# Kernel optimization log

Measured on AMD Instinct MI355X. Metric: run time of the kernel, lower is better.

The kernel has to match this reference:

```python
import jax, jax.numpy as jnp
import numpy as np

B, N, E, D = 4, 50000, 800000, 64


def setup_inputs() -> dict:
    key = jax.random.key(0)
    k_h, k_e, k_w1, k_w2 = jax.random.split(key, 4)
    s = 1.0 / np.sqrt(D)  # glorot-ish scale for 64x64 linear weights
    return {
        "t": jnp.zeros((1,), jnp.float32),
        "h": jax.random.normal(k_h, (B, N, D), jnp.float32),
        "edge_index": jax.random.randint(k_e, (2, E), 0, N, jnp.int32),
        "W1": jax.random.normal(k_w1, (D, D), jnp.float32) * s,
        "b1": jnp.zeros((D,), jnp.float32),
        "W2": jax.random.normal(k_w2, (D, D), jnp.float32) * s,
        "b2": jnp.zeros((D,), jnp.float32),
    }


def _gcn(x, row, col, norm, W, b, n_nodes):
    # x: (B, N, D). PyG GCNConv: linear (no bias) -> normalized gather/scatter -> +bias
    xw = jnp.einsum("bnd,de->bne", x, W)
    msg = xw[:, row, :] * norm[None, :, None]          # (B, E+N, D)
    agg = jax.vmap(lambda m: jax.ops.segment_sum(m, col, num_segments=n_nodes))(msg)
    return agg + b


def reference(t, h, edge_index, W1, b1, W2, b2):
    n_nodes = h.shape[1]
    loop = jnp.arange(n_nodes, dtype=edge_index.dtype)
    # add self-loops (PyG GCNConv default)
    row = jnp.concatenate([edge_index[0], loop])  # source nodes
    col = jnp.concatenate([edge_index[1], loop])  # target nodes
    # symmetric normalization D^{-1/2} (A+I) D^{-1/2}; degree counted on targets
    deg = jax.ops.segment_sum(jnp.ones_like(row, dtype=h.dtype), col, num_segments=n_nodes)
    dis = jnp.where(deg > 0, jax.lax.rsqrt(deg), 0.0)
    norm = dis[row] * dis[col]
    h = jnp.tanh(_gcn(h, row, col, norm, W1, b1, n_nodes))
    h = jnp.tanh(_gcn(h, row, col, norm, W2, b2, n_nodes))
    return h
```

## Files before the change

### kernel.cpp

```cpp
#include <hip/hip_runtime.h>
#include <math.h>

#define B_ 4
#define N_ 50000
#define E_ 800000
#define D_ 64
#define M_ (B_*N_)

typedef _Float16 h4 __attribute__((ext_vector_type(4)));
typedef _Float16 h8 __attribute__((ext_vector_type(8)));
typedef float    f4 __attribute__((ext_vector_type(4)));

__global__ __launch_bounds__(256) void k_count(const int4* __restrict__ col4, int* __restrict__ cnt) {
  int e = blockIdx.x * 256 + threadIdx.x;
  if (e < E_ / 4) {
    int4 c = col4[e];
    atomicAdd(&cnt[c.x], 1);
    atomicAdd(&cnt[c.y], 1);
    atomicAdd(&cnt[c.z], 1);
    atomicAdd(&cnt[c.w], 1);
  }
}

__global__ __launch_bounds__(1024) void k_scan_a(const int* __restrict__ cnt, int* __restrict__ part,
                                                 float* __restrict__ dis) {
  __shared__ int sd[1024];
  int i = blockIdx.x * 1024 + threadIdx.x;
  int v = (i < N_) ? cnt[i] : 0;
  if (i < N_) dis[i] = 1.0f / sqrtf((float)(v + 1));
  sd[threadIdx.x] = v;
  __syncthreads();
  for (int s = 512; s > 0; s >>= 1) {
    if (threadIdx.x < s) sd[threadIdx.x] += sd[threadIdx.x + s];
    __syncthreads();
  }
  if (threadIdx.x == 0) part[blockIdx.x] = sd[0];
}

__global__ __launch_bounds__(1024) void k_scan_c(const int* __restrict__ cnt, const int* __restrict__ part,
                                                 int* __restrict__ off, int* __restrict__ cur) {
  __shared__ int sd[1024];
  __shared__ int base_s;
  int i = blockIdx.x * 1024 + threadIdx.x;
  int v = (i < N_) ? cnt[i] : 0;
  if (threadIdx.x == 0) {
    int b = 0;
    for (int j = 0; j < (int)blockIdx.x; j++) b += part[j];
    base_s = b;
  }
  sd[threadIdx.x] = v;
  __syncthreads();
  for (int s = 1; s < 1024; s <<= 1) {
    int t = (threadIdx.x >= s) ? sd[threadIdx.x - s] : 0;
    __syncthreads();
    sd[threadIdx.x] += t;
    __syncthreads();
  }
  int incl = sd[threadIdx.x];
  if (i < N_) { off[i] = base_s + incl - v; cur[i] = 0; }
  if (i == N_ - 1) off[N_] = base_s + incl;
}

__global__ __launch_bounds__(256) void k_fill(const int* __restrict__ row, const int* __restrict__ col,
                                              const int* __restrict__ off, int* __restrict__ cur,
                                              const float* __restrict__ dis,
                                              int2* __restrict__ em) {
  int e = blockIdx.x * 256 + threadIdx.x;
  if (e < E_) {
    int c = col[e], r = row[e];
    int p = off[c] + atomicAdd(&cur[c], 1);
    float w = dis[r] * dis[c];
    em[p] = make_int2(r << 9, __float_as_int(w));
  }
}

__global__ __launch_bounds__(256) void k_wfrag(const float* __restrict__ W1, const float* __restrict__ W2,
                                               h8* __restrict__ Wf1, h8* __restrict__ Wf2) {
  int t0 = threadIdx.x;
  for (int w = 0; w < 2; w++) {
    const float* W = w ? W2 : W1;
    h8* Wf = w ? Wf2 : Wf1;
    for (int p = 0; p < 2; p++) {
      int fid = p * 256 + t0;
      int khalf = fid >> 8;
      int rem = fid & 255;
      int tt = rem >> 6;
      int lane = rem & 63;
      int kq = lane >> 4, m = lane & 15;
      h8 v;
#pragma unroll
      for (int j = 0; j < 8; j++) {
        int k = khalf * 32 + kq * 8 + j;
        v[j] = (_Float16)W[k * 64 + tt * 16 + m];
      }
      Wf[fid] = v;
    }
  }
}

template<int IN_F16>
__global__ __launch_bounds__(256) void k_linear(const void* __restrict__ Xv,
                                                const h8* __restrict__ Wf,
                                                _Float16* __restrict__ Y) {
  int wv = blockIdx.x * 4 + (threadIdx.x >> 6);
  int lane = threadIdx.x & 63;
  int m = lane & 15, kq = lane >> 4;
  size_t r0 = (size_t)wv * 16;
  h8 a0, a1;
  if constexpr (IN_F16) {
    const _Float16* xr = (const _Float16*)Xv + (r0 + m) * 64 + kq * 8;
    a0 = *(const h8*)(xr);
    a1 = *(const h8*)(xr + 32);
  } else {
    const float* xr = (const float*)Xv + (r0 + m) * 64 + kq * 8;
    f4 f0 = *(const f4*)(xr);
    f4 f1 = *(const f4*)(xr + 4);
    f4 f2 = *(const f4*)(xr + 32);
    f4 f3 = *(const f4*)(xr + 36);
#pragma unroll
    for (int j = 0; j < 4; j++) {
      a0[j] = (_Float16)f0[j]; a0[j + 4] = (_Float16)f1[j];
      a1[j] = (_Float16)f2[j]; a1[j + 4] = (_Float16)f3[j];
    }
  }
  f4 acc[4];
#pragma unroll
  for (int t = 0; t < 4; t++) {
    h8 b0 = Wf[t * 64 + lane];
    h8 b1 = Wf[256 + t * 64 + lane];
    f4 c = {0.f, 0.f, 0.f, 0.f};
    c = __builtin_amdgcn_mfma_f32_16x16x32_f16(a0, b0, c, 0, 0, 0);
    c = __builtin_amdgcn_mfma_f32_16x16x32_f16(a1, b1, c, 0, 0, 0);
    acc[t] = c;
  }
  int b  = (int)(r0 / N_);
  int n0 = (int)(r0 - (size_t)b * N_);
#pragma unroll
  for (int t = 0; t < 4; t++) {
#pragma unroll
    for (int r = 0; r < 4; r++) {
      int n = n0 + kq * 4 + r;
      Y[(size_t)n * 256 + b * 64 + t * 16 + m] = (_Float16)acc[t][r];
    }
  }
}

template<int OUT_F16>
__global__ __launch_bounds__(512) void k_agg(const _Float16* __restrict__ xw,
                                             const int* __restrict__ off,
                                             const int2* __restrict__ em,
                                             const float* __restrict__ bias,
                                             void* __restrict__ outv) {
  int node = blockIdx.x * 8 + (threadIdx.x >> 6);
  int lane = threadIdx.x & 63;
  const char* xb = (const char*)xw + (size_t)(lane * 8);
  int s0 = __builtin_amdgcn_readfirstlane(off[node]);
  int e0 = __builtin_amdgcn_readfirstlane(off[node + 1]);
  float sw = 1.0f / (float)(e0 - s0 + 1);
  h4 sv = *(const h4*)(xb + ((size_t)node << 9));
  f4 acc = __builtin_convertvector(sv, f4) * sw;
#define EDGE_(mm) do { \
    h4 v_ = *(const h4*)(xb + (unsigned)(mm).x); \
    acc += __builtin_convertvector(v_, f4) * __int_as_float((mm).y); \
  } while (0)
  int j = s0;
  for (; j + 8 <= e0; j += 8) {
    int2 m0 = em[j],     m1 = em[j + 1], m2 = em[j + 2], m3 = em[j + 3];
    int2 m4 = em[j + 4], m5 = em[j + 5], m6 = em[j + 6], m7 = em[j + 7];
    EDGE_(m0); EDGE_(m1); EDGE_(m2); EDGE_(m3);
    EDGE_(m4); EDGE_(m5); EDGE_(m6); EDGE_(m7);
  }
  for (; j < e0; ++j) { int2 m = em[j]; EDGE_(m); }
#undef EDGE_
  int b  = lane >> 4;
  int d0 = (lane & 15) * 4;
  f4 bb = *(const f4*)(bias + d0);
  float r0 = tanhf(acc.x + bb.x);
  float r1 = tanhf(acc.y + bb.y);
  float r2 = tanhf(acc.z + bb.z);
  float r3 = tanhf(acc.w + bb.w);
  if constexpr (OUT_F16) {
    h4 o;
    o[0] = (_Float16)r0; o[1] = (_Float16)r1;
    o[2] = (_Float16)r2; o[3] = (_Float16)r3;
    *(h4*)((_Float16*)outv + ((size_t)b * N_ + node) * 64 + d0) = o;
  } else {
    f4 r = {r0, r1, r2, r3};
    *(f4*)((float*)outv + ((size_t)b * N_ + node) * 64 + d0) = r;
  }
}

extern "C" void kernel_launch(void* const* d_in, const int* in_sizes, int n_in,
                              void* d_out, int out_size, void* d_ws, size_t ws_size,
                              hipStream_t stream) {
  const float* h  = (const float*)d_in[1];
  const int*   ei = (const int*)d_in[2];
  const float* W1 = (const float*)d_in[3];
  const float* b1 = (const float*)d_in[4];
  const float* W2 = (const float*)d_in[5];
  const float* b2 = (const float*)d_in[6];
  float* out = (float*)d_out;
  const int* row = ei;
  const int* col = ei + E_;

  char* p = (char*)d_ws;
  _Float16* xw = (_Float16*)p; p += (size_t)M_ * D_ * sizeof(_Float16);
  int2* em  = (int2*)p;   p += (size_t)E_ * sizeof(int2);
  int*  cnt = (int*)p;    p += (size_t)N_ * sizeof(int);
  int*  off = (int*)p;    p += (size_t)(N_ + 4) * sizeof(int);
  int*  cur = (int*)p;    p += (size_t)N_ * sizeof(int);
  float* dis = (float*)p; p += (size_t)N_ * sizeof(float);
  int*  prt = (int*)p;    p += 64 * sizeof(int);
  h8*   Wf1 = (h8*)p;     p += 512 * sizeof(h8);
  h8*   Wf2 = (h8*)p;     p += 512 * sizeof(h8);
  _Float16* h1 = (_Float16*)d_out;

  hipMemsetAsync(cnt, 0, N_ * sizeof(int), stream);

  k_count<<<(E_ / 4 + 255) / 256, 256, 0, stream>>>((const int4*)col, cnt);
  int nscan = (N_ + 1023) / 1024;
  k_scan_a<<<nscan, 1024, 0, stream>>>(cnt, prt, dis);
  k_scan_c<<<nscan, 1024, 0, stream>>>(cnt, prt, off, cur);
  k_fill<<<(E_ + 255) / 256, 256, 0, stream>>>(row, col, off, cur, dis, em);
  k_wfrag<<<1, 256, 0, stream>>>(W1, W2, Wf1, Wf2);

  k_linear<0><<<M_ / 64, 256, 0, stream>>>(h, Wf1, xw);
  k_agg<1><<<N_ / 8, 512, 0, stream>>>(xw, off, em, b1, h1);
  k_linear<1><<<M_ / 64, 256, 0, stream>>>(h1, Wf2, xw);
  k_agg<0><<<N_ / 8, 512, 0, stream>>>(xw, off, em, b2, out);
}
```

Measured before the change: 334.4 us.

## Fold GCN normalization into linear output and pad CSR for per-batch-plane aggregation

The linear kernel now scales each output row by the source node's D^{-1/2}, and the aggregation multiplies by the target's D^{-1/2} at the end. This removes the per-edge weights, so the edge list stores only a 4-byte source offset. The feature buffer moves from node-interleaved batches to one plane per batch, with a zero sentinel row. Each node's edge list is padded to a multiple of 16 with sentinel indices, so the aggregation runs unrolled 16-wide with no tail loop, using one wave per (batch, node) and one fp16 element per lane. The two scan kernels are merged into one that uses an atomic global base, which makes the CSR ordering nondeterministic. The cost is 4x more waves, narrower 2-byte gathers, and extra padded gathers.

```diff
diff --git a/kernel.cpp b/kernel.cpp
--- a/kernel.cpp
+++ b/kernel.cpp
@@ -22,33 +22,18 @@
   }
 }
 
-__global__ __launch_bounds__(1024) void k_scan_a(const int* __restrict__ cnt, int* __restrict__ part,
-                                                 float* __restrict__ dis) {
-  __shared__ int sd[1024];
-  int i = blockIdx.x * 1024 + threadIdx.x;
-  int v = (i < N_) ? cnt[i] : 0;
-  if (i < N_) dis[i] = 1.0f / sqrtf((float)(v + 1));
-  sd[threadIdx.x] = v;
-  __syncthreads();
-  for (int s = 512; s > 0; s >>= 1) {
-    if (threadIdx.x < s) sd[threadIdx.x] += sd[threadIdx.x + s];
-    __syncthreads();
-  }
-  if (threadIdx.x == 0) part[blockIdx.x] = sd[0];
-}
-
-__global__ __launch_bounds__(1024) void k_scan_c(const int* __restrict__ cnt, const int* __restrict__ part,
-                                                 int* __restrict__ off, int* __restrict__ cur) {
+__global__ __launch_bounds__(1024) void k_scan(const int* __restrict__ cnt,
+                                               float* __restrict__ dis,
+                                               int* __restrict__ off, int* __restrict__ cur,
+                                               int* __restrict__ em, int* __restrict__ gbase,
+                                               _Float16* __restrict__ xw) {
   __shared__ int sd[1024];
   __shared__ int base_s;
   int i = blockIdx.x * 1024 + threadIdx.x;
   int v = (i < N_) ? cnt[i] : 0;
-  if (threadIdx.x == 0) {
-    int b = 0;
-    for (int j = 0; j < (int)blockIdx.x; j++) b += part[j];
-    base_s = b;
-  }
-  sd[threadIdx.x] = v;
+  int degp = (v + 15) & ~15;
+  if (i < N_) dis[i] = 1.0f / sqrtf((float)(v + 1));
+  sd[threadIdx.x] = degp;
   __syncthreads();
   for (int s = 1; s < 1024; s <<= 1) {
     int t = (threadIdx.x >= s) ? sd[threadIdx.x - s] : 0;
@@ -56,21 +41,29 @@
     sd[threadIdx.x] += t;
     __syncthreads();
   }
-  int incl = sd[threadIdx.x];
-  if (i < N_) { off[i] = base_s + incl - v; cur[i] = 0; }
-  if (i == N_ - 1) off[N_] = base_s + incl;
+  if (threadIdx.x == 1023) base_s = atomicAdd(gbase, sd[1023]);
+  __syncthreads();
+  int o = base_s + sd[threadIdx.x] - degp;
+  if (i < N_) {
+    off[i] = o;
+    cur[i] = 0;
+    for (int k = v; k < degp; k++) em[o + k] = N_ * 128;
+  }
+  if (blockIdx.x == 0 && threadIdx.x < 32) {
+    int pl = threadIdx.x >> 3, q = threadIdx.x & 7;
+    h8 z = {};
+    *(h8*)((char*)xw + (size_t)pl * (N_ + 1) * 128 + (size_t)N_ * 128 + q * 16) = z;
+  }
 }
 
 __global__ __launch_bounds__(256) void k_fill(const int* __restrict__ row, const int* __restrict__ col,
                                               const int* __restrict__ off, int* __restrict__ cur,
-                                              const float* __restrict__ dis,
-                                              int2* __restrict__ em) {
+                                              int* __restrict__ em) {
   int e = blockIdx.x * 256 + threadIdx.x;
   if (e < E_) {
     int c = col[e], r = row[e];
     int p = off[c] + atomicAdd(&cur[c], 1);
-    float w = dis[r] * dis[c];
-    em[p] = make_int2(r << 9, __float_as_int(w));
+    em[p] = r << 7;
   }
 }
 
@@ -101,6 +94,7 @@
 template<int IN_F16>
 __global__ __launch_bounds__(256) void k_linear(const void* __restrict__ Xv,
                                                 const h8* __restrict__ Wf,
+                                                const float* __restrict__ dis,
                                                 _Float16* __restrict__ Y) {
   int wv = blockIdx.x * 4 + (threadIdx.x >> 6);
   int lane = threadIdx.x & 63;
@@ -135,12 +129,15 @@
   }
   int b  = (int)(r0 / N_);
   int n0 = (int)(r0 - (size_t)b * N_);
+  float dv[4];
+#pragma unroll
+  for (int rr = 0; rr < 4; rr++) dv[rr] = dis[n0 + kq * 4 + rr];
+  size_t ybase = ((size_t)b * (N_ + 1) + n0) * 64;
 #pragma unroll
   for (int t = 0; t < 4; t++) {
 #pragma unroll
-    for (int r = 0; r < 4; r++) {
-      int n = n0 + kq * 4 + r;
-      Y[(size_t)n * 256 + b * 64 + t * 16 + m] = (_Float16)acc[t][r];
+    for (int rr = 0; rr < 4; rr++) {
+      Y[ybase + (size_t)(kq * 4 + rr) * 64 + t * 16 + m] = (_Float16)(acc[t][rr] * dv[rr]);
     }
   }
 }
@@ -148,45 +145,35 @@
 template<int OUT_F16>
 __global__ __launch_bounds__(512) void k_agg(const _Float16* __restrict__ xw,
                                              const int* __restrict__ off,
-                                             const int2* __restrict__ em,
+                                             const int* __restrict__ cnt,
+                                             const int* __restrict__ em,
                                              const float* __restrict__ bias,
                                              void* __restrict__ outv) {
-  int node = blockIdx.x * 8 + (threadIdx.x >> 6);
+  int wid = __builtin_amdgcn_readfirstlane(blockIdx.x * 8 + (threadIdx.x >> 6));
   int lane = threadIdx.x & 63;
-  const char* xb = (const char*)xw + (size_t)(lane * 8);
-  int s0 = __builtin_amdgcn_readfirstlane(off[node]);
-  int e0 = __builtin_amdgcn_readfirstlane(off[node + 1]);
-  float sw = 1.0f / (float)(e0 - s0 + 1);
-  h4 sv = *(const h4*)(xb + ((size_t)node << 9));
-  f4 acc = __builtin_convertvector(sv, f4) * sw;
-#define EDGE_(mm) do { \
-    h4 v_ = *(const h4*)(xb + (unsigned)(mm).x); \
-    acc += __builtin_convertvector(v_, f4) * __int_as_float((mm).y); \
-  } while (0)
-  int j = s0;
-  for (; j + 8 <= e0; j += 8) {
-    int2 m0 = em[j],     m1 = em[j + 1], m2 = em[j + 2], m3 = em[j + 3];
-    int2 m4 = em[j + 4], m5 = em[j + 5], m6 = em[j + 6], m7 = em[j + 7];
-    EDGE_(m0); EDGE_(m1); EDGE_(m2); EDGE_(m3);
-    EDGE_(m4); EDGE_(m5); EDGE_(m6); EDGE_(m7);
-  }
-  for (; j < e0; ++j) { int2 m = em[j]; EDGE_(m); }
-#undef EDGE_
-  int b  = lane >> 4;
-  int d0 = (lane & 15) * 4;
-  f4 bb = *(const f4*)(bias + d0);
-  float r0 = tanhf(acc.x + bb.x);
-  float r1 = tanhf(acc.y + bb.y);
-  float r2 = tanhf(acc.z + bb.z);
-  float r3 = tanhf(acc.w + bb.w);
+  int b    = (int)((unsigned)wid / N_);
+  int node = wid - b * N_;
+  const char* plane = (const char*)xw + (size_t)b * (N_ + 1) * 128 + (size_t)(lane * 2);
+  int s0   = __builtin_amdgcn_readfirstlane(off[node]);
+  int deg  = __builtin_amdgcn_readfirstlane(cnt[node]);
+  int degp = (deg + 15) & ~15;
+  float dc = 1.0f / sqrtf((float)(deg + 1));
+  float acc = (float)*(const _Float16*)(plane + (size_t)node * 128);
+  for (int j = s0; j < s0 + degp; j += 16) {
+    int o[16];
+#pragma unroll
+    for (int k = 0; k < 16; k++) o[k] = em[j + k];
+    _Float16 v[16];
+#pragma unroll
+    for (int k = 0; k < 16; k++) v[k] = *(const _Float16*)(plane + (unsigned)o[k]);
+#pragma unroll
+    for (int k = 0; k < 16; k++) acc += (float)v[k];
+  }
+  float r = tanhf(acc * dc + bias[lane]);
   if constexpr (OUT_F16) {
-    h4 o;
-    o[0] = (_Float16)r0; o[1] = (_Float16)r1;
-    o[2] = (_Float16)r2; o[3] = (_Float16)r3;
-    *(h4*)((_Float16*)outv + ((size_t)b * N_ + node) * 64 + d0) = o;
+    ((_Float16*)outv)[((size_t)b * N_ + node) * 64 + lane] = (_Float16)r;
   } else {
-    f4 r = {r0, r1, r2, r3};
-    *(f4*)((float*)outv + ((size_t)b * N_ + node) * 64 + d0) = r;
+    ((float*)outv)[((size_t)b * N_ + node) * 64 + lane] = r;
   }
 }
 
@@ -204,28 +191,27 @@
   const int* col = ei + E_;
 
   char* p = (char*)d_ws;
-  _Float16* xw = (_Float16*)p; p += (size_t)M_ * D_ * sizeof(_Float16);
-  int2* em  = (int2*)p;   p += (size_t)E_ * sizeof(int2);
+  _Float16* xw = (_Float16*)p; p += (size_t)B_ * (N_ + 1) * 64 * sizeof(_Float16);
+  int*  em  = (int*)p;    p += (size_t)(E_ + 15 * N_ + 64) * sizeof(int);
   int*  cnt = (int*)p;    p += (size_t)N_ * sizeof(int);
-  int*  off = (int*)p;    p += (size_t)(N_ + 4) * sizeof(int);
+  int*  gbase = (int*)p;  p += 4 * sizeof(int);
+  int*  off = (int*)p;    p += (size_t)N_ * sizeof(int);
   int*  cur = (int*)p;    p += (size_t)N_ * sizeof(int);
   float* dis = (float*)p; p += (size_t)N_ * sizeof(float);
-  int*  prt = (int*)p;    p += 64 * sizeof(int);
   h8*   Wf1 = (h8*)p;     p += 512 * sizeof(h8);
   h8*   Wf2 = (h8*)p;     p += 512 * sizeof(h8);
   _Float16* h1 = (_Float16*)d_out;
 
-  hipMemsetAsync(cnt, 0, N_ * sizeof(int), stream);
+  hipMemsetAsync(cnt, 0, (N_ + 1) * sizeof(int), stream);
 
   k_count<<<(E_ / 4 + 255) / 256, 256, 0, stream>>>((const int4*)col, cnt);
   int nscan = (N_ + 1023) / 1024;
-  k_scan_a<<<nscan, 1024, 0, stream>>>(cnt, prt, dis);
-  k_scan_c<<<nscan, 1024, 0, stream>>>(cnt, prt, off, cur);
-  k_fill<<<(E_ + 255) / 256, 256, 0, stream>>>(row, col, off, cur, dis, em);
+  k_scan<<<nscan, 1024, 0, stream>>>(cnt, dis, off, cur, em, gbase, xw);
+  k_fill<<<(E_ + 255) / 256, 256, 0, stream>>>(row, col, off, cur, em);
   k_wfrag<<<1, 256, 0, stream>>>(W1, W2, Wf1, Wf2);
 
-  k_linear<0><<<M_ / 64, 256, 0, stream>>>(h, Wf1, xw);
-  k_agg<1><<<N_ / 8, 512, 0, stream>>>(xw, off, em, b1, h1);
-  k_linear<1><<<M_ / 64, 256, 0, stream>>>(h1, Wf2, xw);
-  k_agg<0><<<N_ / 8, 512, 0, stream>>>(xw, off, em, b2, out);
-}
+  k_linear<0><<<M_ / 64, 256, 0, stream>>>(h, Wf1, dis, xw);
+  k_agg<1><<<(B_ * N_) / 8, 512, 0, stream>>>(xw, off, cnt, em, b1, h1);
+  k_linear<1><<<M_ / 64, 256, 0, stream>>>(h1, Wf2, dis, xw);
+  k_agg<0><<<(B_ * N_) / 8, 512, 0, stream>>>(xw, off, cnt, em, b2, out);
+}
```

New measurement: 363.1 us. 8.6% more time.

## Fuse preprocessing launches and overlap CSR fill with first linear layer

Applied to the files above, without the earlier changes.

Cuts the pipeline from nine launches to six. The weight-fragment conversion is folded into extra blocks of the count kernel. The two-pass scan is replaced by a single scan that takes each block's base offset from a global atomic counter. The edge-fill scatter and the first dense linear run as separate block ranges of one kernel, so they can overlap. Aggregation now takes each node's degree from the count array, because the atomic-ordered block bases no longer keep offsets monotone. That ordering also shuffles the CSR layout slightly, which could change memory locality.

```diff
diff --git a/kernel.cpp b/kernel.cpp
--- a/kernel.cpp
+++ b/kernel.cpp
@@ -7,11 +7,35 @@
 #define D_ 64
 #define M_ (B_*N_)
 
+#define LIN_BLKS_ (M_/64)
+#define FILL_BLKS_ ((E_+255)/256)
+#define CNT_BLKS_ ((E_/4+255)/256)
+
 typedef _Float16 h4 __attribute__((ext_vector_type(4)));
 typedef _Float16 h8 __attribute__((ext_vector_type(8)));
 typedef float    f4 __attribute__((ext_vector_type(4)));
 
-__global__ __launch_bounds__(256) void k_count(const int4* __restrict__ col4, int* __restrict__ cnt) {
+__device__ __forceinline__ void wfrag_one(const float* __restrict__ W, h8* __restrict__ Wf, int fid) {
+  int khalf = fid >> 8, rem = fid & 255, tt = rem >> 6, lane = rem & 63;
+  int kq = lane >> 4, m = lane & 15;
+  h8 v;
+#pragma unroll
+  for (int j = 0; j < 8; j++) {
+    int k = khalf * 32 + kq * 8 + j;
+    v[j] = (_Float16)W[k * 64 + tt * 16 + m];
+  }
+  Wf[fid] = v;
+}
+
+__global__ __launch_bounds__(256) void k_count(const int4* __restrict__ col4, int* __restrict__ cnt,
+                                               const float* __restrict__ W1, const float* __restrict__ W2,
+                                               h8* __restrict__ Wf1, h8* __restrict__ Wf2) {
+  if (blockIdx.x >= CNT_BLKS_) {
+    int fa = (blockIdx.x - CNT_BLKS_) * 256 + threadIdx.x;
+    if (fa < 512) wfrag_one(W1, Wf1, fa);
+    else          wfrag_one(W2, Wf2, fa - 512);
+    return;
+  }
   int e = blockIdx.x * 256 + threadIdx.x;
   if (e < E_ / 4) {
     int4 c = col4[e];
@@ -22,32 +46,15 @@
   }
 }
 
-__global__ __launch_bounds__(1024) void k_scan_a(const int* __restrict__ cnt, int* __restrict__ part,
-                                                 float* __restrict__ dis) {
-  __shared__ int sd[1024];
-  int i = blockIdx.x * 1024 + threadIdx.x;
-  int v = (i < N_) ? cnt[i] : 0;
-  if (i < N_) dis[i] = 1.0f / sqrtf((float)(v + 1));
-  sd[threadIdx.x] = v;
-  __syncthreads();
-  for (int s = 512; s > 0; s >>= 1) {
-    if (threadIdx.x < s) sd[threadIdx.x] += sd[threadIdx.x + s];
-    __syncthreads();
-  }
-  if (threadIdx.x == 0) part[blockIdx.x] = sd[0];
-}
-
-__global__ __launch_bounds__(1024) void k_scan_c(const int* __restrict__ cnt, const int* __restrict__ part,
-                                                 int* __restrict__ off, int* __restrict__ cur) {
+__global__ __launch_bounds__(1024) void k_scan(const int* __restrict__ cnt,
+                                               float* __restrict__ dis,
+                                               int* __restrict__ off, int* __restrict__ cur,
+                                               int* __restrict__ gbase) {
   __shared__ int sd[1024];
   __shared__ int base_s;
   int i = blockIdx.x * 1024 + threadIdx.x;
   int v = (i < N_) ? cnt[i] : 0;
-  if (threadIdx.x == 0) {
-    int b = 0;
-    for (int j = 0; j < (int)blockIdx.x; j++) b += part[j];
-    base_s = b;
-  }
+  if (i < N_) dis[i] = 1.0f / sqrtf((float)(v + 1));
   sd[threadIdx.x] = v;
   __syncthreads();
   for (int s = 1; s < 1024; s <<= 1) {
@@ -56,54 +63,17 @@
     sd[threadIdx.x] += t;
     __syncthreads();
   }
-  int incl = sd[threadIdx.x];
-  if (i < N_) { off[i] = base_s + incl - v; cur[i] = 0; }
-  if (i == N_ - 1) off[N_] = base_s + incl;
-}
-
-__global__ __launch_bounds__(256) void k_fill(const int* __restrict__ row, const int* __restrict__ col,
-                                              const int* __restrict__ off, int* __restrict__ cur,
-                                              const float* __restrict__ dis,
-                                              int2* __restrict__ em) {
-  int e = blockIdx.x * 256 + threadIdx.x;
-  if (e < E_) {
-    int c = col[e], r = row[e];
-    int p = off[c] + atomicAdd(&cur[c], 1);
-    float w = dis[r] * dis[c];
-    em[p] = make_int2(r << 9, __float_as_int(w));
-  }
-}
-
-__global__ __launch_bounds__(256) void k_wfrag(const float* __restrict__ W1, const float* __restrict__ W2,
-                                               h8* __restrict__ Wf1, h8* __restrict__ Wf2) {
-  int t0 = threadIdx.x;
-  for (int w = 0; w < 2; w++) {
-    const float* W = w ? W2 : W1;
-    h8* Wf = w ? Wf2 : Wf1;
-    for (int p = 0; p < 2; p++) {
-      int fid = p * 256 + t0;
-      int khalf = fid >> 8;
-      int rem = fid & 255;
-      int tt = rem >> 6;
-      int lane = rem & 63;
-      int kq = lane >> 4, m = lane & 15;
-      h8 v;
-#pragma unroll
-      for (int j = 0; j < 8; j++) {
-        int k = khalf * 32 + kq * 8 + j;
-        v[j] = (_Float16)W[k * 64 + tt * 16 + m];
-      }
-      Wf[fid] = v;
-    }
+  if (threadIdx.x == 1023) base_s = atomicAdd(gbase, sd[1023]);
+  __syncthreads();
+  if (i < N_) {
+    off[i] = base_s + sd[threadIdx.x] - v;
+    cur[i] = 0;
   }
 }
 
 template<int IN_F16>
-__global__ __launch_bounds__(256) void k_linear(const void* __restrict__ Xv,
-                                                const h8* __restrict__ Wf,
-                                                _Float16* __restrict__ Y) {
-  int wv = blockIdx.x * 4 + (threadIdx.x >> 6);
-  int lane = threadIdx.x & 63;
+__device__ __forceinline__ void linear_wave(const void* __restrict__ Xv, const h8* __restrict__ Wf,
+                                            _Float16* __restrict__ Y, int wv, int lane) {
   int m = lane & 15, kq = lane >> 4;
   size_t r0 = (size_t)wv * 16;
   h8 a0, a1;
@@ -145,18 +115,45 @@
   }
 }
 
+__global__ __launch_bounds__(256) void k_fill_lin1(const int* __restrict__ row, const int* __restrict__ col,
+                                                   const int* __restrict__ off, int* __restrict__ cur,
+                                                   const float* __restrict__ dis, int2* __restrict__ em,
+                                                   const float* __restrict__ h, const h8* __restrict__ Wf1,
+                                                   _Float16* __restrict__ xw) {
+  if (blockIdx.x < LIN_BLKS_) {
+    int wv = blockIdx.x * 4 + (threadIdx.x >> 6);
+    linear_wave<0>(h, Wf1, xw, wv, threadIdx.x & 63);
+    return;
+  }
+  int e = (blockIdx.x - LIN_BLKS_) * 256 + threadIdx.x;
+  if (e < E_) {
+    int c = col[e], r = row[e];
+    int p = off[c] + atomicAdd(&cur[c], 1);
+    float w = dis[r] * dis[c];
+    em[p] = make_int2(r << 9, __float_as_int(w));
+  }
+}
+
+__global__ __launch_bounds__(256) void k_linear2(const _Float16* __restrict__ X, const h8* __restrict__ Wf,
+                                                 _Float16* __restrict__ Y) {
+  int wv = blockIdx.x * 4 + (threadIdx.x >> 6);
+  linear_wave<1>(X, Wf, Y, wv, threadIdx.x & 63);
+}
+
 template<int OUT_F16>
 __global__ __launch_bounds__(512) void k_agg(const _Float16* __restrict__ xw,
                                              const int* __restrict__ off,
+                                             const int* __restrict__ cnt,
                                              const int2* __restrict__ em,
                                              const float* __restrict__ bias,
                                              void* __restrict__ outv) {
   int node = blockIdx.x * 8 + (threadIdx.x >> 6);
   int lane = threadIdx.x & 63;
   const char* xb = (const char*)xw + (size_t)(lane * 8);
-  int s0 = __builtin_amdgcn_readfirstlane(off[node]);
-  int e0 = __builtin_amdgcn_readfirstlane(off[node + 1]);
-  float sw = 1.0f / (float)(e0 - s0 + 1);
+  int s0  = __builtin_amdgcn_readfirstlane(off[node]);
+  int deg = __builtin_amdgcn_readfirstlane(cnt[node]);
+  int e0  = s0 + deg;
+  float sw = 1.0f / (float)(deg + 1);
   h4 sv = *(const h4*)(xb + ((size_t)node << 9));
   f4 acc = __builtin_convertvector(sv, f4) * sw;
 #define EDGE_(mm) do { \
@@ -170,7 +167,7 @@
     EDGE_(m0); EDGE_(m1); EDGE_(m2); EDGE_(m3);
     EDGE_(m4); EDGE_(m5); EDGE_(m6); EDGE_(m7);
   }
-  for (; j < e0; ++j) { int2 m = em[j]; EDGE_(m); }
+  for (; j < e0; ++j) { int2 mm = em[j]; EDGE_(mm); }
 #undef EDGE_
   int b  = lane >> 4;
   int d0 = (lane & 15) * 4;
@@ -207,25 +204,20 @@
   _Float16* xw = (_Float16*)p; p += (size_t)M_ * D_ * sizeof(_Float16);
   int2* em  = (int2*)p;   p += (size_t)E_ * sizeof(int2);
   int*  cnt = (int*)p;    p += (size_t)N_ * sizeof(int);
-  int*  off = (int*)p;    p += (size_t)(N_ + 4) * sizeof(int);
+  int*  gbase = (int*)p;  p += 4 * sizeof(int);
+  int*  off = (int*)p;    p += (size_t)N_ * sizeof(int);
   int*  cur = (int*)p;    p += (size_t)N_ * sizeof(int);
   float* dis = (float*)p; p += (size_t)N_ * sizeof(float);
-  int*  prt = (int*)p;    p += 64 * sizeof(int);
   h8*   Wf1 = (h8*)p;     p += 512 * sizeof(h8);
   h8*   Wf2 = (h8*)p;     p += 512 * sizeof(h8);
   _Float16* h1 = (_Float16*)d_out;
 
-  hipMemsetAsync(cnt, 0, N_ * sizeof(int), stream);
-
-  k_count<<<(E_ / 4 + 255) / 256, 256, 0, stream>>>((const int4*)col, cnt);
-  int nscan = (N_ + 1023) / 1024;
-  k_scan_a<<<nscan, 1024, 0, stream>>>(cnt, prt, dis);
-  k_scan_c<<<nscan, 1024, 0, stream>>>(cnt, prt, off, cur);
-  k_fill<<<(E_ + 255) / 256, 256, 0, stream>>>(row, col, off, cur, dis, em);
-  k_wfrag<<<1, 256, 0, stream>>>(W1, W2, Wf1, Wf2);
-
-  k_linear<0><<<M_ / 64, 256, 0, stream>>>(h, Wf1, xw);
-  k_agg<1><<<N_ / 8, 512, 0, stream>>>(xw, off, em, b1, h1);
-  k_linear<1><<<M_ / 64, 256, 0, stream>>>(h1, Wf2, xw);
-  k_agg<0><<<N_ / 8, 512, 0, stream>>>(xw, off, em, b2, out);
-}
+  hipMemsetAsync(cnt, 0, (N_ + 4) * sizeof(int), stream);
+
+  k_count<<<CNT_BLKS_ + 4, 256, 0, stream>>>((const int4*)col, cnt, W1, W2, Wf1, Wf2);
+  k_scan<<<(N_ + 1023) / 1024, 1024, 0, stream>>>(cnt, dis, off, cur, gbase);
+  k_fill_lin1<<<LIN_BLKS_ + FILL_BLKS_, 256, 0, stream>>>(row, col, off, cur, dis, em, h, Wf1, xw);
+  k_agg<1><<<N_ / 8, 512, 0, stream>>>(xw, off, cnt, em, b1, h1);
+  k_linear2<<<M_ / 64, 256, 0, stream>>>(h1, Wf2, xw);
+  k_agg<0><<<N_ / 8, 512, 0, stream>>>(xw, off, cnt, em, b2, out);
+}
```

Result: faster. 326.1 us (-2.5%).
